# Kernel tuning notes

Measured on AMD Instinct MI355X. Metric: run time of the kernel, lower is better.

The kernel has to match this reference:

```python
import jax, jax.numpy as jnp
import numpy as np

# ---- model dims ----
D_MODEL = 256; D_STATE = 128; D_CONV = 4; EXPAND = 2; HEADDIM = 64
D_INNER = EXPAND * D_MODEL            # 512
NHEADS = D_INNER // HEADDIM           # 8
CONV_DIM = D_INNER + 2 * D_STATE      # 768
D_IN_PROJ = 2 * D_INNER + 2 * D_STATE + NHEADS  # 1288
N_GENES = 4095; BATCH = 4; CHUNK = 64
GENE_ID_DIM = 64; PATH_DIM = 128; CHR_DIM = 16; N_CHROM = 25; LFF = 32
GENE_FEAT_DIM = GENE_ID_DIM + PATH_DIM + 2 * CHR_DIM  # 224
N_PERT = 2048; PERT_DIM = 128


def silu(x):
    return x * jax.nn.sigmoid(x)


def segsum_exp(a):
    # a: (..., T). Returns lower-triangular exp(sum_{k=j+1..i} a_k), zero above diag.
    T = a.shape[-1]
    cs = jnp.cumsum(a, axis=-1)
    d = cs[..., :, None] - cs[..., None, :]
    mask = jnp.tril(jnp.ones((T, T), dtype=bool))
    return jnp.exp(jnp.where(mask, d, 0.0)) * mask


def ssd(X, A, B, C):
    # Chunked SSD (Mamba2 selective scan). X:(b,l,h,p) pre-multiplied by dt,
    # A:(b,l,h) = a*dt, B/C:(b,l,n) (ngroups=1 broadcast over heads).
    b, l, h, p = X.shape
    n = B.shape[-1]
    c = l // CHUNK
    Xc = X.reshape(b, c, CHUNK, h, p)
    Bc = B.reshape(b, c, CHUNK, n)
    Cc = C.reshape(b, c, CHUNK, n)
    Ac = A.reshape(b, c, CHUNK, h).transpose(0, 3, 1, 2)  # (b,h,c,cl)
    A_cs = jnp.cumsum(Ac, axis=-1)
    L = segsum_exp(Ac)                                     # (b,h,c,cl,cl)
    Y_diag = jnp.einsum('bcln,bcsn,bhcls,bcshp->bclhp', Cc, Bc, L, Xc)
    decay_states = jnp.exp(A_cs[..., -1:] - A_cs)          # (b,h,c,cl)
    states = jnp.einsum('bcln,bhcl,bclhp->bchpn', Bc, decay_states, Xc)
    chunk_decay = jnp.exp(A_cs[..., -1])                   # (b,h,c)

    def step(h_prev, inp):
        dec, s = inp
        return h_prev * dec[..., None, None] + s, h_prev

    init = jnp.zeros((b, h, p, n), X.dtype)
    _, prev = jax.lax.scan(step, init, (chunk_decay.transpose(2, 0, 1),
                                        states.transpose(1, 0, 2, 3, 4)))
    prev = prev.transpose(1, 0, 2, 3, 4)                   # (b,c,h,p,n)
    Y_off = jnp.einsum('bcln,bchpn,bhcl->bclhp', Cc, prev, jnp.exp(A_cs))
    return (Y_diag + Y_off).reshape(b, l, h, p)


def mamba2(x, in_w, conv_w, conv_b, dt_bias, A_log, D, norm_w, out_w):
    b, l, _ = x.shape
    zxbcdt = x @ in_w.T                                    # (b,l,1288)
    z = zxbcdt[..., :D_INNER]
    xBC = zxbcdt[..., D_INNER:D_INNER + CONV_DIM]
    dt = jax.nn.softplus(zxbcdt[..., D_INNER + CONV_DIM:] + dt_bias)  # (b,l,h)
    # causal depthwise conv1d
    xc = jax.lax.conv_general_dilated(
        xBC.transpose(0, 2, 1), conv_w[:, None, :], (1,), [(D_CONV - 1, 0)],
        feature_group_count=CONV_DIM,
        dimension_numbers=('NCH', 'OIH', 'NCH'))
    xBC = silu(xc.transpose(0, 2, 1) + conv_b)
    xs = xBC[..., :D_INNER].reshape(b, l, NHEADS, HEADDIM)
    Bm = xBC[..., D_INNER:D_INNER + D_STATE]
    Cm = xBC[..., D_INNER + D_STATE:]
    A = -jnp.exp(A_log)                                    # (h,)
    y = ssd(xs * dt[..., None], dt * A, Bm, Cm) + D[:, None] * xs
    y = y.reshape(b, l, D_INNER)
    y = y * silu(z)                                        # gated RMSNorm
    y = y * jax.lax.rsqrt(jnp.mean(y * y, axis=-1, keepdims=True) + 1e-5) * norm_w
    return y @ out_w.T


def _forward(perturbation_idx, chr_idx, locus_fourier, pathway_features,
             gene_id_emb, chr_emb, locus_w, locus_b, pert_emb, cond_w, cond_b,
             inp_w, inp_b, ln_g, ln_b,
             mf_in_w, mf_conv_w, mf_conv_b, mf_dt_bias, mf_A_log, mf_D, mf_norm_w, mf_out_w,
             mb_in_w, mb_conv_w, mb_conv_b, mb_dt_bias, mb_A_log, mb_D, mb_norm_w, mb_out_w,
             head_w, head_b):
    e_locus = jax.nn.gelu(locus_fourier @ locus_w.T + locus_b, approximate=False)
    gene_feat = jnp.concatenate(
        [gene_id_emb, pathway_features, chr_emb[chr_idx], e_locus], axis=-1)  # (G,224)
    cond = pert_emb[perturbation_idx] @ cond_w.T + cond_b                      # (B,224)
    seq = jnp.concatenate(
        [cond[:, None, :],
         jnp.broadcast_to(gene_feat[None], (BATCH, N_GENES, GENE_FEAT_DIM))], axis=1)
    seq = seq @ inp_w.T + inp_b                                                # (B,4096,256)
    mu = jnp.mean(seq, axis=-1, keepdims=True)
    var = jnp.var(seq, axis=-1, keepdims=True)
    seq = (seq - mu) * jax.lax.rsqrt(var + 1e-5) * ln_g + ln_b
    # L = 4096 is already a multiple of 16 -> no padding branch.
    h_fwd = mamba2(seq, mf_in_w, mf_conv_w, mf_conv_b, mf_dt_bias, mf_A_log, mf_D, mf_norm_w, mf_out_w)
    h_bwd = jnp.flip(mamba2(jnp.flip(seq, 1), mb_in_w, mb_conv_w, mb_conv_b, mb_dt_bias, mb_A_log, mb_D, mb_norm_w, mb_out_w), 1)
    H = h_fwd + h_bwd
    return H[:, 1:, :] @ head_w.T + head_b                                     # (B,4095,1)


def setup_inputs() -> dict:
    key = jax.random.key(0)
    ks = iter(jax.random.split(key, 64))

    def nrm(shape, s=0.02):
        return jax.random.normal(next(ks), shape, jnp.float32) * s

    inp = {}
    inp['perturbation_idx'] = jax.random.randint(next(ks), (BATCH,), 0, N_PERT)
    inp['chr_idx'] = jax.random.randint(next(ks), (N_GENES,), 0, N_CHROM)
    inp['locus_fourier'] = nrm((N_GENES, 2 * LFF), 1.0)
    inp['pathway_features'] = nrm((N_GENES, PATH_DIM), 1.0)
    inp['gene_id_emb'] = nrm((N_GENES, GENE_ID_DIM))
    inp['chr_emb'] = nrm((N_CHROM, CHR_DIM))
    inp['locus_w'] = nrm((CHR_DIM, 2 * LFF)); inp['locus_b'] = jnp.zeros((CHR_DIM,))
    inp['pert_emb'] = nrm((N_PERT, PERT_DIM))
    inp['cond_w'] = nrm((GENE_FEAT_DIM, PERT_DIM)); inp['cond_b'] = jnp.zeros((GENE_FEAT_DIM,))
    inp['inp_w'] = nrm((D_MODEL, GENE_FEAT_DIM)); inp['inp_b'] = jnp.zeros((D_MODEL,))
    inp['ln_g'] = jnp.ones((D_MODEL,)); inp['ln_b'] = jnp.zeros((D_MODEL,))
    for pre in ('mf_', 'mb_'):
        inp[pre + 'in_w'] = nrm((D_IN_PROJ, D_MODEL))
        inp[pre + 'conv_w'] = nrm((CONV_DIM, D_CONV), 0.2)
        inp[pre + 'conv_b'] = jnp.zeros((CONV_DIM,))
        inp[pre + 'dt_bias'] = nrm((NHEADS,), 0.5)
        inp[pre + 'A_log'] = jnp.log(jax.random.uniform(next(ks), (NHEADS,), jnp.float32, 1.0, 16.0))
        inp[pre + 'D'] = jnp.ones((NHEADS,))
        inp[pre + 'norm_w'] = jnp.ones((D_INNER,))
        inp[pre + 'out_w'] = nrm((D_MODEL, D_INNER))
    inp['head_w'] = nrm((1, D_MODEL)); inp['head_b'] = jnp.zeros((1,))
    return inp


def reference(perturbation_idx, chr_idx, locus_fourier, pathway_features,
              gene_id_emb, chr_emb, locus_w, locus_b, pert_emb, cond_w, cond_b,
              inp_w, inp_b, ln_g, ln_b,
              mf_in_w, mf_conv_w, mf_conv_b, mf_dt_bias, mf_A_log, mf_D, mf_norm_w, mf_out_w,
              mb_in_w, mb_conv_w, mb_conv_b, mb_dt_bias, mb_A_log, mb_D, mb_norm_w, mb_out_w,
              head_w, head_b):
    return _forward(perturbation_idx, chr_idx, locus_fourier, pathway_features,
                    gene_id_emb, chr_emb, locus_w, locus_b, pert_emb, cond_w, cond_b,
                    inp_w, inp_b, ln_g, ln_b,
                    mf_in_w, mf_conv_w, mf_conv_b, mf_dt_bias, mf_A_log, mf_D, mf_norm_w, mf_out_w,
                    mb_in_w, mb_conv_w, mb_conv_b, mb_dt_bias, mb_A_log, mb_D, mb_norm_w, mb_out_w,
                    head_w, head_b)
```

## Files before the change

kernel.cpp:

```cpp
#include <hip/hip_runtime.h>
#include <hip/hip_bf16.h>
#include <math.h>

#define LSEQ   4096
#define NGENES 4095
#define NB     4
#define DM     256
#define DI     512
#define DST    128
#define NH     8
#define HD     64
#define CONVD  768
#define DIP    1288
#define NCHK   64
#define CHK    64
#define GFD    224

#define ZN  ((size_t)NB*LSEQ*DI)
#define XN  ((size_t)NB*LSEQ*CONVD)
#define DN  ((size_t)NB*LSEQ*NH)
#define AN  ((size_t)NB*NH*LSEQ)
#define SN  ((size_t)NB*NCHK*NH*HD*DST)
#define GN  ((size_t)NB*NCHK*CHK*CHK)
#define BTN ((size_t)NB*NCHK*DST*CHK)
#define HN  ((size_t)NB*LSEQ*DM)

typedef short bf16x8 __attribute__((ext_vector_type(8)));
typedef short bf16x4 __attribute__((ext_vector_type(4)));
typedef float f32x4 __attribute__((ext_vector_type(4)));

__device__ __forceinline__ float bf2f(unsigned short u){
    unsigned int x = ((unsigned int)u) << 16;
    return __uint_as_float(x);
}
__device__ __forceinline__ unsigned short f2bf(float f){
    __hip_bfloat16 h = __float2bfloat16(f);
    return *reinterpret_cast<unsigned short*>(&h);
}

typedef const __attribute__((address_space(1))) void* gas_t;
typedef __attribute__((address_space(3))) void* las_t;
__device__ __forceinline__ void gload16(const void* g, void* l){
    __builtin_amdgcn_global_load_lds((gas_t)g, (las_t)l, 16, 0, 0);
}

__global__ void k_detect(const unsigned int* p, int* flag){
    *flag = (*p == 0x3F803F80u) ? 1 : 0;
}

struct ConvAll { const void* src[31]; float* dst[31]; int n[31]; };
__global__ void k_convert_all(ConvAll a, const int* flag){
    int ai = blockIdx.y;
    int n = a.n[ai];
    const void* s = a.src[ai]; float* d = a.dst[ai];
    bool bf = (*flag != 0);
    for(int i = blockIdx.x*256 + threadIdx.x; i < n; i += gridDim.x*256){
        d[i] = bf ? bf2f(((const unsigned short*)s)[i]) : ((const float*)s)[i];
    }
}

struct PackAll { const void* src[4]; unsigned short* dst[4]; int n[4]; };
__global__ void k_pack_all(PackAll a, const int* flag){
    int ai = blockIdx.y;
    int n = a.n[ai];
    const void* s = a.src[ai]; unsigned short* d = a.dst[ai];
    bool bf = (*flag != 0);
    for(int i = blockIdx.x*256 + threadIdx.x; i < n; i += gridDim.x*256){
        if(bf) d[i] = ((const unsigned short*)s)[i];
        else   d[i] = f2bf(((const float*)s)[i]);
    }
}

__global__ void k_packw256(const void* src, unsigned short* dst, const int* flag){
    int row = blockIdx.x, col = threadIdx.x;
    unsigned short v = 0;
    if(col < GFD){
        if(*flag) v = ((const unsigned short*)src)[row*GFD + col];
        else      v = f2bf(((const float*)src)[row*GFD + col]);
    }
    dst[row*256 + col] = v;
}

__global__ void k_genefeat(const float* gene_id, const float* pathway, const float* chr_emb,
                           const int* chr_idx, const float* lf, const float* locus_w,
                           const float* locus_b, unsigned short* gfb){
    int g = blockIdx.x; int t = threadIdx.x;
    float v = 0.f;
    if(t < 64)       v = gene_id[g*64 + t];
    else if(t < 192) v = pathway[g*128 + (t-64)];
    else if(t < 208) v = chr_emb[chr_idx[g]*16 + (t-192)];
    else if(t < 224){
        int j = t - 208;
        float acc = locus_b[j];
        for(int k=0;k<64;k++) acc += lf[g*64+k]*locus_w[j*64+k];
        v = 0.5f*acc*(1.0f + erff(acc*0.7071067811865475f));
    }
    gfb[g*256 + t] = f2bf(v);
}

__global__ void k_cond(const int* pidx, const float* pert_emb, const float* cond_w,
                       const float* cond_b, unsigned short* condb){
    int b = blockIdx.x, t = threadIdx.x;
    float acc = 0.f;
    if(t < GFD){
        const float* pe = pert_emb + pidx[b]*128;
        acc = cond_b[t];
        for(int k=0;k<128;k++) acc += pe[k]*cond_w[t*128+k];
    }
    condb[b*256 + t] = f2bf(acc);
}

__global__ __launch_bounds__(256) void k_mm_seqpre(const unsigned short* gfb,
            const unsigned short* condb, const unsigned short* Wb,
            const float* inp_b, float* seq_pre){
    __shared__ unsigned short sh[16384];
    int sblk = (blockIdx.x & 7)*32 + (blockIdx.x >> 3);
    int bm = sblk>>1, bn = sblk&1;
    int m0 = bm*128, n0 = bn*128;
    int t = threadIdx.x, lane = t&63;
    int wid = t>>6, wm = wid>>1, wn = wid&1;
    int fr = lane&15, fk = lane>>4;
    int srow = t>>3;
    int scol = ((t&7) ^ (srow&7))*8;
    const unsigned short* gA[4]; const unsigned short* gB[4];
#pragma unroll
    for(int q=0;q<4;q++){
        int row = q*32 + srow;
        int m = m0+row; int b = m>>12, l = m&4095;
        gA[q] = l ? &gfb[(size_t)(l-1)*256 + scol] : &condb[(size_t)b*256 + scol];
        gB[q] = &Wb[(size_t)(n0+row)*256 + scol];
    }
    unsigned short* lA = &sh[t*8];
    unsigned short* lB = &sh[8192 + t*8];
    f32x4 acc[4][4];
#pragma unroll
    for(int i=0;i<4;i++)
#pragma unroll
        for(int j=0;j<4;j++) acc[i][j] = (f32x4){0.f,0.f,0.f,0.f};
    for(int it=0; it<4; it++){
#pragma unroll
        for(int q=0;q<4;q++){
            gload16(gA[q], lA + q*2048);
            gload16(gB[q], lB + q*2048);
            gA[q] += 64; gB[q] += 64;
        }
        __syncthreads();
#pragma unroll
        for(int kk8=0;kk8<8;kk8+=4){
            bf16x8 av[4], bv[4];
#pragma unroll
            for(int i=0;i<4;i++){
                int r = wm*64+i*16+fr;
                av[i] = *(bf16x8*)&sh[r*64 + (((kk8+fk)^(r&7))*8)];
            }
#pragma unroll
            for(int j=0;j<4;j++){
                int r = wn*64+j*16+fr;
                bv[j] = *(bf16x8*)&sh[8192 + r*64 + (((kk8+fk)^(r&7))*8)];
            }
#pragma unroll
            for(int i=0;i<4;i++)
#pragma unroll
                for(int j=0;j<4;j++)
                    acc[i][j] = __builtin_amdgcn_mfma_f32_16x16x32_bf16(av[i], bv[j], acc[i][j], 0,0,0);
        }
        __syncthreads();
    }
#pragma unroll
    for(int i=0;i<4;i++)
#pragma unroll
        for(int rr=0;rr<4;rr++){
            int m = m0 + wm*64 + i*16 + fk*4 + rr;
#pragma unroll
            for(int j=0;j<4;j++){
                int n = n0 + wn*64 + j*16 + fr;
                seq_pre[(size_t)m*256 + n] = acc[i][j][rr] + inp_b[n];
            }
        }
}

__global__ void k_ln(const float* seq_pre, const float* ln_g, const float* ln_b,
                     unsigned short* seqb){
    int t = threadIdx.x; int w = t>>6, lane = t&63;
    int m = blockIdx.x*4 + w;
    f32x4 v = *(const f32x4*)&seq_pre[(size_t)m*256 + lane*4];
    float s1 = v[0]+v[1]+v[2]+v[3];
    float s2 = v[0]*v[0]+v[1]*v[1]+v[2]*v[2]+v[3]*v[3];
#pragma unroll
    for(int o=32;o>0;o>>=1){ s1 += __shfl_xor(s1,o,64); s2 += __shfl_xor(s2,o,64); }
    float mu  = s1*(1.f/256.f);
    float var = s2*(1.f/256.f) - mu*mu;
    float rs = rsqrtf(var+1e-5f);
    unsigned short o4[4];
#pragma unroll
    for(int j=0;j<4;j++){
        int n = lane*4+j;
        o4[j] = f2bf((v[j]-mu)*rs*ln_g[n] + ln_b[n]);
    }
    *(unsigned long long*)&seqb[(size_t)m*256 + lane*4] = *(unsigned long long*)o4;
}

__global__ __launch_bounds__(256) void k_mm_inproj(const unsigned short* seqb,
            const unsigned short* W0, const unsigned short* W1,
            const float* dtb0, const float* dtb1,
            unsigned short* zbase, unsigned short* xbase, float* dtbase){
    __shared__ unsigned short sh[16384];
    int blk = (blockIdx.x & 7)*352 + (blockIdx.x >> 3);
    int dir = blk >= 1408; int inner = blk - dir*1408;
    int bm = inner/11, bn = inner%11;
    int m0 = bm*128, n0 = bn*128;
    const unsigned short* Wb = dir ? W1 : W0;
    const float* dt_bias = dir ? dtb1 : dtb0;
    unsigned short* zb   = zbase + (size_t)dir*ZN;
    unsigned short* xbcr = xbase + (size_t)dir*XN;
    float* dtb = dtbase + (size_t)dir*DN;
    int t = threadIdx.x, lane = t&63;
    int wid = t>>6, wm = wid>>1, wn = wid&1;
    int fr = lane&15, fk = lane>>4;
    int srow = t>>3;
    int scol = ((t&7) ^ (srow&7))*8;
    const unsigned short* gA[4]; const unsigned short* gB[4];
#pragma unroll
    for(int q=0;q<4;q++){
        int row = q*32 + srow;
        int m = m0+row; int b = m>>12, l = m&4095;
        int ml = dir ? (4095-l) : l;
        gA[q] = &seqb[(size_t)(b*4096+ml)*256 + scol];
        gB[q] = &Wb[(size_t)(n0+row)*256 + scol];
    }
    unsigned short* lA = &sh[t*8];
    unsigned short* lB = &sh[8192 + t*8];
    f32x4 acc[4][4];
#pragma unroll
    for(int i=0;i<4;i++)
#pragma unroll
        for(int j=0;j<4;j++) acc[i][j] = (f32x4){0.f,0.f,0.f,0.f};
    for(int it=0; it<4; it++){
#pragma unroll
        for(int q=0;q<4;q++){
            gload16(gA[q], lA + q*2048);
            gload16(gB[q], lB + q*2048);
            gA[q] += 64; gB[q] += 64;
        }
        __syncthreads();
#pragma unroll
        for(int kk8=0;kk8<8;kk8+=4){
            bf16x8 av[4], bv[4];
#pragma unroll
            for(int i=0;i<4;i++){
                int r = wm*64+i*16+fr;
                av[i] = *(bf16x8*)&sh[r*64 + (((kk8+fk)^(r&7))*8)];
            }
#pragma unroll
            for(int j=0;j<4;j++){
                int r = wn*64+j*16+fr;
                bv[j] = *(bf16x8*)&sh[8192 + r*64 + (((kk8+fk)^(r&7))*8)];
            }
#pragma unroll
            for(int i=0;i<4;i++)
#pragma unroll
                for(int j=0;j<4;j++)
                    acc[i][j] = __builtin_amdgcn_mfma_f32_16x16x32_bf16(av[i], bv[j], acc[i][j], 0,0,0);
        }
        __syncthreads();
    }
    if(bn == 10){
#pragma unroll
        for(int i=0;i<4;i++)
#pragma unroll
            for(int rr=0;rr<4;rr++){
                int m = m0 + wm*64 + i*16 + fk*4 + rr;
#pragma unroll
                for(int j=0;j<4;j++){
                    int n = n0 + wn*64 + j*16 + fr;
                    if(n >= DIP) continue;
                    int hh = n - 1280;
                    float x = acc[i][j][rr] + dt_bias[hh];
                    dtb[(size_t)m*NH + hh] = (x > 20.f) ? x : log1pf(expf(x));
                }
            }
        return;
    }
    unsigned short* dst; int stride, coff;
    if(bn < 4){ dst = zb;   stride = DI;    coff = bn*128; }
    else      { dst = xbcr; stride = CONVD; coff = bn*128 - 512; }
#pragma unroll
    for(int p=0;p<2;p++){
        if(wm == p){
#pragma unroll
            for(int i=0;i<4;i++)
#pragma unroll
                for(int j=0;j<4;j++)
#pragma unroll
                    for(int rr=0;rr<4;rr++){
                        int row = i*16 + fk*4 + rr;
                        int col = wn*64 + j*16 + fr;
                        sh[row*136 + col] = f2bf(acc[i][j][rr]);
                    }
        }
        __syncthreads();
#pragma unroll
        for(int k=0;k<4;k++){
            int idx = t + k*256;
            int row = idx>>4, c8 = (idx&15)*8;
            bf16x8 v = *(bf16x8*)&sh[row*136 + c8];
            *(bf16x8*)&dst[(size_t)(m0+p*64+row)*stride + coff + c8] = v;
        }
        __syncthreads();
    }
}

__global__ __launch_bounds__(256) void k_conv(const unsigned short* xbase,
        const float* cw0, const float* cw1, const float* cb0, const float* cb1,
        unsigned short* obase){
    __shared__ unsigned short raw[19*768];
    __shared__ float cwf[4*768];
    __shared__ float cbf[768];
    int blk = blockIdx.x;
    int dir = blk>>10; int rem = blk&1023;
    int b = rem>>8, rg = rem&255;
    const unsigned short* xr = xbase + (size_t)dir*XN;
    unsigned short* out = obase + (size_t)dir*XN;
    const float* cw = dir ? cw1 : cw0;
    const float* cb = dir ? cb1 : cb0;
    int l0 = rg*16;
    int t = threadIdx.x;
    for(int i=t;i<3072;i+=256){ int q=i/768, c=i%768; cwf[q*768+c] = cw[c*4+q]; }
    for(int i=t;i<768;i+=256) cbf[i] = cb[i];
    for(int i=t;i<19*96;i+=256){
        int r = i/96, c8 = (i%96)*8;
        int l = l0 - 3 + r;
        bf16x8 v = (bf16x8){0,0,0,0,0,0,0,0};
        if(l >= 0) v = *(const bf16x8*)&xr[(size_t)(b*4096+l)*768 + c8];
        *(bf16x8*)&raw[r*768 + c8] = v;
    }
    __syncthreads();
    for(int i=t;i<16*96;i+=256){
        int r = i/96, c8 = (i%96)*8;
        bf16x8 o;
#pragma unroll
        for(int j=0;j<8;j++){
            int c = c8+j;
            float acc = cbf[c];
#pragma unroll
            for(int q=0;q<4;q++) acc += cwf[q*768+c]*bf2f(raw[(r+q)*768 + c]);
            o[j] = (short)f2bf(acc/(1.f+expf(-acc)));
        }
        *(bf16x8*)&out[(size_t)(b*4096+l0+r)*768 + c8] = o;
    }
}

__global__ void k_cumsum(const float* dtbase, const float* Al0, const float* Al1,
                         float* acsbase){
    __shared__ float tmp[64];
    int blk = blockIdx.x;
    int dir = blk>>11; int rem = blk&2047;
    int c = rem & 63; int bh = rem >> 6; int h = bh & 7; int b = bh >> 3;
    const float* dtb = dtbase + (size_t)dir*DN;
    float* acs = acsbase + (size_t)dir*AN;
    int s = threadIdx.x;
    float A = -expf((dir?Al1:Al0)[h]);
    int l = c*64 + s;
    tmp[s] = dtb[(size_t)(b*4096+l)*NH + h] * A;
    __syncthreads();
    if(s == 0){ for(int i=1;i<64;i++) tmp[i] += tmp[i-1]; }
    __syncthreads();
    acs[(size_t)(b*8+h)*4096 + l] = tmp[s];
}

__global__ __launch_bounds__(256) void k_cbprep(const unsigned short* xbase,
        unsigned short* Gbase, unsigned short* BTbase){
    __shared__ unsigned short Bb[64][136];
    __shared__ unsigned short Cb[64][136];
    __shared__ unsigned short BTs[128][72];
    int blk = blockIdx.x;
    int dir = blk>>8; int bc = blk&255;
    int b = bc>>6, c = bc&63;
    const unsigned short* xbcb = xbase + (size_t)dir*XN;
    unsigned short* Gb = Gbase + (size_t)dir*GN;
    unsigned short* BTg = BTbase + (size_t)dir*BTN;
    int t = threadIdx.x, lane = t&63, wid = t>>6;
    int fr = lane&15, fk = lane>>4;
    size_t rowbase = (size_t)(b*4096 + c*64)*CONVD;
#pragma unroll
    for(int q=0;q<4;q++){
        int e = t + q*256; int r = e>>4, ch = (e&15)*8;
        *(bf16x8*)&Bb[r][ch] = *(const bf16x8*)&xbcb[rowbase + (size_t)r*CONVD + 512 + ch];
        *(bf16x8*)&Cb[r][ch] = *(const bf16x8*)&xbcb[rowbase + (size_t)r*CONVD + 640 + ch];
    }
    __syncthreads();
    f32x4 g[4];
#pragma unroll
    for(int j=0;j<4;j++) g[j] = (f32x4){0.f,0.f,0.f,0.f};
#pragma unroll
    for(int k0=0;k0<128;k0+=32){
        bf16x8 av = *(bf16x8*)&Cb[wid*16+fr][k0+fk*8];
#pragma unroll
        for(int j=0;j<4;j++){
            bf16x8 bv = *(bf16x8*)&Bb[j*16+fr][k0+fk*8];
            g[j] = __builtin_amdgcn_mfma_f32_16x16x32_bf16(av, bv, g[j], 0,0,0);
        }
    }
    size_t gbase = (size_t)bc*4096;
#pragma unroll
    for(int j=0;j<4;j++)
#pragma unroll
        for(int rr=0;rr<4;rr++)
            Gb[gbase + (size_t)(wid*16+fk*4+rr)*64 + j*16+fr] = f2bf(g[j][rr]);
#pragma unroll
    for(int q=0;q<4;q++){
        int e = t + q*256; int s = e>>4, n0 = (e&15)*8;
        bf16x8 v = *(bf16x8*)&Bb[s][n0];
#pragma unroll
        for(int j=0;j<8;j++){
            int n = n0 + j;
            BTs[n][s ^ (n&56)] = (unsigned short)v[j];
        }
    }
    __syncthreads();
    size_t btbase = (size_t)bc*8192;
#pragma unroll
    for(int q=0;q<4;q++){
        int e = t + q*256; int n = e>>3, s0 = (e&7)*8;
        bf16x8 v = *(bf16x8*)&BTs[n][s0 ^ (n&56)];
        *(bf16x8*)&BTg[btbase + (size_t)n*64 + s0] = v;
    }
}

__global__ __launch_bounds__(256) void k_ssd_intra(const unsigned short* xbase,
        const unsigned short* Gbase, const unsigned short* BTbase,
        const float* dtbase, const float* acsbase,
        const float* Dv0, const float* Dv1,
        unsigned short* Ybase, unsigned short* sbase_){
    __shared__ unsigned short Gs[64][72];
    __shared__ unsigned short Ms[64][72];
    __shared__ unsigned short XT[64][72];
    __shared__ unsigned short BTs[128][72];
    __shared__ float acs_s[64], dts[64], ws[64];
    int blk = blockIdx.x;
    int dir = blk>>9; int rem = blk&511;
    int hg = rem&1, c = (rem>>1)&63, b = rem>>7;
    int bc = b*64 + c;
    const unsigned short* xbcb = xbase + (size_t)dir*XN;
    const unsigned short* Gb = Gbase + (size_t)dir*GN;
    const unsigned short* BTg = BTbase + (size_t)dir*BTN;
    const float* dtb = dtbase + (size_t)dir*DN;
    const float* acs = acsbase + (size_t)dir*AN;
    const float* Dv = dir ? Dv1 : Dv0;
    unsigned short* Yb = Ybase + (size_t)dir*XN;
    unsigned short* states = sbase_ + (size_t)dir*SN;
    int t = threadIdx.x, lane = t&63, wid = t>>6;
    int wr = wid>>1, wc = wid&1;
    int fr = lane&15, fk = lane>>4;
    size_t rowbase = (size_t)(b*4096 + c*64)*CONVD;
    size_t gbase = (size_t)bc*4096;
    size_t btbase = (size_t)bc*8192;
#pragma unroll
    for(int q=0;q<2;q++){
        int e = t + q*256; int l = e>>3, s0 = (e&7)*8;
        *(bf16x8*)&Gs[l][s0] = *(const bf16x8*)&Gb[gbase + (size_t)l*64 + s0];
    }
#pragma unroll
    for(int q=0;q<4;q++){
        int e = t + q*256; int n = e>>3, s0 = (e&7)*8;
        *(bf16x8*)&BTs[n][s0 ^ (n&56)] = *(const bf16x8*)&BTg[btbase + (size_t)n*64 + s0];
    }
    for(int hh=0; hh<4; hh++){
        int h = hg*4 + hh;
        __syncthreads();
#pragma unroll
        for(int q=0;q<2;q++){
            int e = t + q*256; int s = e>>3, p0 = (e&7)*8;
            bf16x8 v = *(const bf16x8*)&xbcb[rowbase + (size_t)s*CONVD + h*64 + p0];
            int sw = s ^ (p0&56);
#pragma unroll
            for(int j=0;j<8;j++) XT[p0+j][sw] = (unsigned short)v[j];
        }
        if(t < 64){
            acs_s[t] = acs[(size_t)(b*8+h)*4096 + c*64 + t];
            dts[t]   = dtb[(size_t)(b*4096 + c*64 + t)*NH + h];
        }
        __syncthreads();
        if(t < 64) ws[t] = expf(acs_s[63]-acs_s[t])*dts[t];
#pragma unroll
        for(int q=0;q<16;q++){
            int e = t + q*256; int l = e>>6, s = e&63;
            float m = (s <= l) ? bf2f(Gs[l][s])*expf(acs_s[l]-acs_s[s])*dts[s] : 0.f;
            Ms[l][s] = f2bf(m);
        }
        __syncthreads();
        f32x4 y[2][2];
#pragma unroll
        for(int i=0;i<2;i++)
#pragma unroll
            for(int j=0;j<2;j++) y[i][j] = (f32x4){0.f,0.f,0.f,0.f};
#pragma unroll
        for(int k0=0;k0<64;k0+=32){
            bf16x8 av[2], bv[2];
#pragma unroll
            for(int i=0;i<2;i++) av[i] = *(bf16x8*)&Ms[wr*32+i*16+fr][k0+fk*8];
#pragma unroll
            for(int j=0;j<2;j++){
                int p = wc*32+j*16+fr;
                bv[j] = *(bf16x8*)&XT[p][(k0+fk*8) ^ (p&56)];
            }
#pragma unroll
            for(int i=0;i<2;i++)
#pragma unroll
                for(int j=0;j<2;j++)
                    y[i][j] = __builtin_amdgcn_mfma_f32_16x16x32_bf16(av[i], bv[j], y[i][j], 0,0,0);
        }
        float Dh = Dv[h];
#pragma unroll
        for(int i=0;i<2;i++)
#pragma unroll
            for(int j=0;j<2;j++)
#pragma unroll
                for(int rr=0;rr<4;rr++){
                    int l = wr*32 + i*16 + fk*4 + rr;
                    int p = wc*32 + j*16 + fr;
                    float xv = bf2f(XT[p][l ^ (p&56)]);
                    Yb[(size_t)(b*4096 + c*64 + l)*DI + h*64 + p] = f2bf(y[i][j][rr] + Dh*xv);
                }
        f32x4 s4[2][4];
#pragma unroll
        for(int i=0;i<2;i++)
#pragma unroll
            for(int j=0;j<4;j++) s4[i][j] = (f32x4){0.f,0.f,0.f,0.f};
#pragma unroll
        for(int k0=0;k0<64;k0+=32){
            bf16x8 av[2], bv[4];
#pragma unroll
            for(int i=0;i<2;i++){
                int p = wr*32+i*16+fr;
                bf16x8 raw = *(bf16x8*)&XT[p][(k0+fk*8) ^ (p&56)];
#pragma unroll
                for(int e=0;e<8;e++) av[i][e] = (short)f2bf(bf2f((unsigned short)raw[e]) * ws[k0+fk*8+e]);
            }
#pragma unroll
            for(int j=0;j<4;j++){
                int n = wc*64+j*16+fr;
                bv[j] = *(bf16x8*)&BTs[n][(k0+fk*8) ^ (n&56)];
            }
#pragma unroll
            for(int i=0;i<2;i++)
#pragma unroll
                for(int j=0;j<4;j++)
                    s4[i][j] = __builtin_amdgcn_mfma_f32_16x16x32_bf16(av[i], bv[j], s4[i][j], 0,0,0);
        }
        size_t sb = ((size_t)bc*8 + h)*8192;
#pragma unroll
        for(int i=0;i<2;i++)
#pragma unroll
            for(int j=0;j<4;j++)
#pragma unroll
                for(int rr=0;rr<4;rr++){
                    int p = wr*32 + i*16 + fk*4 + rr;
                    int n = wc*64 + j*16 + fr;
                    states[sb + p*128 + n] = f2bf(s4[i][j][rr]);
                }
    }
}

__global__ void k_scan(unsigned short* sbase_, const float* acsbase){
    __shared__ float dec_s[64];
    int blk = blockIdx.x;
    int dir = blk>>8; int rem = blk&255;
    int e8 = rem&7, h = (rem>>3)&7, b = rem>>6;
    unsigned short* states = sbase_ + (size_t)dir*SN;
    const float* acs = acsbase + (size_t)dir*AN;
    int t = threadIdx.x;
    if(t < 64) dec_s[t] = expf(acs[(size_t)(b*8+h)*4096 + t*64 + 63]);
    __syncthreads();
    int off = e8*1024 + t*4;
    float h4[4] = {0.f,0.f,0.f,0.f};
    size_t base0 = ((size_t)(b*64)*8 + h)*8192 + off;
    for(int c0=0;c0<64;c0+=4){
        bf16x4 v[4];
#pragma unroll
        for(int u=0;u<4;u++)
            v[u] = *(const bf16x4*)&states[base0 + (size_t)(c0+u)*65536];
#pragma unroll
        for(int u=0;u<4;u++){
            float dec = dec_s[c0+u];
            bf16x4 o;
#pragma unroll
            for(int j=0;j<4;j++){
                o[j] = (short)f2bf(h4[j]);
                h4[j] = h4[j]*dec + bf2f((unsigned short)v[u][j]);
            }
            *(bf16x4*)&states[base0 + (size_t)(c0+u)*65536] = o;
        }
    }
}

__global__ __launch_bounds__(256) void k_ssd_off(const unsigned short* xbase,
        const unsigned short* sbase_, const float* acsbase, unsigned short* Ybase){
    __shared__ unsigned short Ct[64][136];
    __shared__ unsigned short Pv[64][136];
    __shared__ float acs_s[64];
    int blk = blockIdx.x;
    int dir = blk>>8; int bc = blk&255;
    int c = bc&63, b = bc>>6;
    const unsigned short* xbcb = xbase + (size_t)dir*XN;
    const unsigned short* prev = sbase_ + (size_t)dir*SN;
    const float* acs = acsbase + (size_t)dir*AN;
    unsigned short* Yb = Ybase + (size_t)dir*XN;
    int t = threadIdx.x, lane = t&63, wid = t>>6;
    int wr = wid>>1, wc = wid&1;
    int fr = lane&15, fk = lane>>4;
    size_t rowbase = (size_t)(b*4096 + c*64)*CONVD;
#pragma unroll
    for(int q=0;q<4;q++){
        int e = t + q*256;
        int r = e>>4, ch = (e&15)*8;
        *(bf16x8*)&Ct[r][ch] = *(const bf16x8*)&xbcb[rowbase + (size_t)r*CONVD + 640 + ch];
    }
    for(int h=0; h<8; h++){
        size_t sb = ((size_t)bc*8 + h)*8192;
        __syncthreads();
#pragma unroll
        for(int q=0;q<4;q++){
            int e = t + q*256;
            int r = e>>4, ch = (e&15)*8;
            *(bf16x8*)&Pv[r][ch] = *(const bf16x8*)&prev[sb + (size_t)r*128 + ch];
        }
        if(t < 64) acs_s[t] = acs[(size_t)(b*8+h)*4096 + c*64 + t];
        __syncthreads();
        f32x4 o[2][2];
#pragma unroll
        for(int i=0;i<2;i++)
#pragma unroll
            for(int j=0;j<2;j++) o[i][j] = (f32x4){0.f,0.f,0.f,0.f};
        for(int k0=0;k0<128;k0+=32){
            bf16x8 av[2], bv[2];
#pragma unroll
            for(int i=0;i<2;i++) av[i] = *(bf16x8*)&Ct[wr*32+i*16+fr][k0+fk*8];
#pragma unroll
            for(int j=0;j<2;j++) bv[j] = *(bf16x8*)&Pv[wc*32+j*16+fr][k0+fk*8];
#pragma unroll
            for(int i=0;i<2;i++)
#pragma unroll
                for(int j=0;j<2;j++)
                    o[i][j] = __builtin_amdgcn_mfma_f32_16x16x32_bf16(av[i], bv[j], o[i][j], 0,0,0);
        }
#pragma unroll
        for(int i=0;i<2;i++)
#pragma unroll
            for(int j=0;j<2;j++)
#pragma unroll
                for(int rr=0;rr<4;rr++){
                    int l = wr*32 + i*16 + fk*4 + rr;
                    int p = wc*32 + j*16 + fr;
                    size_t yi = (size_t)(b*4096 + c*64 + l)*DI + h*64 + p;
                    float cur = bf2f(Yb[yi]);
                    Yb[yi] = f2bf(cur + o[i][j][rr]*expf(acs_s[l]));
                }
    }
}

__global__ void k_gate(const unsigned short* Ybase, const unsigned short* zbase,
                       const float* nw0, const float* nw1, unsigned short* ynbase){
    int blk = blockIdx.x;
    int dir = blk>>12;
    int t = threadIdx.x; int w = t>>6, lane = t&63;
    int m = (blk&4095)*4 + w;
    const unsigned short* Yb = Ybase + (size_t)dir*XN;
    const unsigned short* zb = zbase + (size_t)dir*ZN;
    unsigned short* ynb = ynbase + (size_t)dir*SN;
    const float* norm_w = dir ? nw1 : nw0;
    size_t base = (size_t)m*DI + lane*8;
    bf16x8 yv = *(const bf16x8*)&Yb[base];
    bf16x8 zv = *(const bf16x8*)&zb[base];
    float v[8]; float ss = 0.f;
#pragma unroll
    for(int j=0;j<8;j++){
        float zf = bf2f((unsigned short)zv[j]);
        float f = bf2f((unsigned short)yv[j]) * (zf/(1.f+expf(-zf)));
        v[j] = f; ss += f*f;
    }
#pragma unroll
    for(int o=32;o>0;o>>=1) ss += __shfl_xor(ss,o,64);
    float r = rsqrtf(ss*(1.f/512.f) + 1e-5f);
    bf16x8 o8;
#pragma unroll
    for(int j=0;j<8;j++) o8[j] = (short)f2bf(v[j]*r*norm_w[lane*8+j]);
    *(bf16x8*)&ynb[base] = o8;
}

__global__ __launch_bounds__(256) void k_mm_outproj(const unsigned short* ynbase,
            const unsigned short* W0, const unsigned short* W1, float* Hbase){
    __shared__ unsigned short sh[16384];
    int blk = (blockIdx.x & 7)*64 + (blockIdx.x >> 3);
    int dir = blk>>8; int rem = blk&255;
    int bm = rem>>1, bn = rem&1;
    int m0 = bm*128, n0 = bn*128;
    const unsigned short* ynb = ynbase + (size_t)dir*SN;
    const unsigned short* Wb = dir ? W1 : W0;
    float* H = Hbase + (size_t)dir*HN;
    int t = threadIdx.x, lane = t&63;
    int wid = t>>6, wm = wid>>1, wn = wid&1;
    int fr = lane&15, fk = lane>>4;
    int srow = t>>3;
    int scol = ((t&7) ^ (srow&7))*8;
    const unsigned short* gA[4]; const unsigned short* gB[4];
#pragma unroll
    for(int q=0;q<4;q++){
        int row = q*32 + srow;
        gA[q] = &ynb[(size_t)(m0+row)*512 + scol];
        gB[q] = &Wb[(size_t)(n0+row)*512 + scol];
    }
    unsigned short* lA = &sh[t*8];
    unsigned short* lB = &sh[8192 + t*8];
    f32x4 acc[4][4];
#pragma unroll
    for(int i=0;i<4;i++)
#pragma unroll
        for(int j=0;j<4;j++) acc[i][j] = (f32x4){0.f,0.f,0.f,0.f};
    for(int it=0; it<8; it++){
#pragma unroll
        for(int q=0;q<4;q++){
            gload16(gA[q], lA + q*2048);
            gload16(gB[q], lB + q*2048);
            gA[q] += 64; gB[q] += 64;
        }
        __syncthreads();
#pragma unroll
        for(int kk8=0;kk8<8;kk8+=4){
            bf16x8 av[4], bv[4];
#pragma unroll
            for(int i=0;i<4;i++){
                int r = wm*64+i*16+fr;
                av[i] = *(bf16x8*)&sh[r*64 + (((kk8+fk)^(r&7))*8)];
            }
#pragma unroll
            for(int j=0;j<4;j++){
                int r = wn*64+j*16+fr;
                bv[j] = *(bf16x8*)&sh[8192 + r*64 + (((kk8+fk)^(r&7))*8)];
            }
#pragma unroll
            for(int i=0;i<4;i++)
#pragma unroll
                for(int j=0;j<4;j++)
                    acc[i][j] = __builtin_amdgcn_mfma_f32_16x16x32_bf16(av[i], bv[j], acc[i][j], 0,0,0);
        }
        __syncthreads();
    }
#pragma unroll
    for(int i=0;i<4;i++)
#pragma unroll
        for(int rr=0;rr<4;rr++){
            int m = m0 + wm*64 + i*16 + fk*4 + rr;
            int b = m>>12, l = m&4095;
            int ml = dir ? (4095 - l) : l;
#pragma unroll
            for(int j=0;j<4;j++){
                int n = n0 + wn*64 + j*16 + fr;
                H[(size_t)(b*4096+ml)*256 + n] = acc[i][j][rr];
            }
        }
}

__global__ void k_head(const float* H0, const float* H1, const float* head_w,
                       const float* head_b, void* out, const int* flag){
    int t = threadIdx.x; int w = t>>6, lane = t&63;
    int row = blockIdx.x*4 + w;
    int b = row/4095, g = row - b*4095;
    size_t idx = ((size_t)(b*4096) + g + 1)*256 + lane*4;
    f32x4 h0 = *(const f32x4*)&H0[idx];
    f32x4 h1 = *(const f32x4*)&H1[idx];
    f32x4 wv = *(const f32x4*)&head_w[lane*4];
    float ss = (h0[0]+h1[0])*wv[0]+(h0[1]+h1[1])*wv[1]+(h0[2]+h1[2])*wv[2]+(h0[3]+h1[3])*wv[3];
#pragma unroll
    for(int o=32;o>0;o>>=1) ss += __shfl_xor(ss,o,64);
    if(lane == 0){
        float val = ss + head_b[0];
        if(*flag) ((__hip_bfloat16*)out)[b*4095 + g] = __float2bfloat16(val);
        else      ((float*)out)[b*4095 + g] = val;
    }
}

extern "C" void kernel_launch(void* const* d_in, const int* in_sizes, int n_in,
                              void* d_out, int out_size, void* d_ws, size_t ws_size,
                              hipStream_t stream){
    if(n_in < 33){
        hipMemsetAsync(d_out, 0, (size_t)out_size*2, stream);
        return;
    }
    char* base = (char*)d_ws;
    size_t off = 256;
    int* flag = (int*)base;
    auto alloc = [&](size_t nbytes)->char*{
        char* p = base + off;
        off += ((nbytes + 255) & ~(size_t)255);
        return p;
    };
    float* F[33];
    for(int i=0;i<33;i++){
        if(i==0 || i==1 || i==11 || i==15 || i==22 || i==23 || i==30){ F[i] = nullptr; continue; }
        F[i] = (float*)alloc((size_t)in_sizes[i]*4);
    }
    unsigned short* inwb[2];
    unsigned short* outwb[2];
    inwb[0]  = (unsigned short*)alloc((size_t)DIP*DM*2);
    inwb[1]  = (unsigned short*)alloc((size_t)DIP*DM*2);
    outwb[0] = (unsigned short*)alloc((size_t)DM*DI*2);
    outwb[1] = (unsigned short*)alloc((size_t)DM*DI*2);
    unsigned short* inpwb = (unsigned short*)alloc((size_t)DM*256*2);
    unsigned short* gfb   = (unsigned short*)alloc((size_t)NGENES*256*2);
    unsigned short* condb = (unsigned short*)alloc((size_t)NB*256*2);
    unsigned short* seqb  = (unsigned short*)alloc((size_t)NB*LSEQ*DM*2);
    float* H0      = (float*)alloc(HN*4);
    float* H1      = (float*)alloc(HN*4);
    unsigned short* zb   = (unsigned short*)alloc(ZN*2*2);
    unsigned short* xbcr = (unsigned short*)alloc(XN*2*2);
    unsigned short* xbcb = (unsigned short*)alloc(XN*2*2);
    float* dtb     = (float*)alloc(DN*2*4);
    float* acs     = (float*)alloc(AN*2*4);
    unsigned short* states = (unsigned short*)alloc(SN*2*2);
    unsigned short* Gb  = (unsigned short*)H0;
    unsigned short* BTg = (unsigned short*)((char*)H0 + ((GN*2*2 + 255) & ~(size_t)255));
    float* seq_pre = (float*)xbcr;
    unsigned short* Ybuf = xbcr;
    unsigned short* ynb = states;
    if(off > ws_size){
        hipMemsetAsync(d_out, 0, (size_t)out_size*2, stream);
        return;
    }

    k_detect<<<1,1,0,stream>>>((const unsigned int*)d_in[13], flag);

    ConvAll ca;
    for(int i=2;i<33;i++){
        int ai = i-2;
        ca.src[ai] = d_in[i];
        ca.dst[ai] = F[i];
        int n = in_sizes[i];
        if(i==11 || i==15 || i==22 || i==23 || i==30) n = 0;
        ca.n[ai] = n;
    }
    k_convert_all<<<dim3(96,31),256,0,stream>>>(ca, flag);

    PackAll pa;
    pa.src[0] = d_in[15]; pa.dst[0] = inwb[0];  pa.n[0] = DIP*DM;
    pa.src[1] = d_in[23]; pa.dst[1] = inwb[1];  pa.n[1] = DIP*DM;
    pa.src[2] = d_in[22]; pa.dst[2] = outwb[0]; pa.n[2] = DM*DI;
    pa.src[3] = d_in[30]; pa.dst[3] = outwb[1]; pa.n[3] = DM*DI;
    k_pack_all<<<dim3(64,4),256,0,stream>>>(pa, flag);
    k_packw256<<<DM,256,0,stream>>>(d_in[11], inpwb, flag);

    k_genefeat<<<NGENES,256,0,stream>>>(F[4], F[3], F[5], (const int*)d_in[1],
                                        F[2], F[6], F[7], gfb);
    k_cond<<<NB,256,0,stream>>>((const int*)d_in[0], F[8], F[9], F[10], condb);
    k_mm_seqpre<<<128*2,256,0,stream>>>(gfb, condb, inpwb, F[12], seq_pre);
    k_ln<<<NB*LSEQ/4,256,0,stream>>>(seq_pre, F[13], F[14], seqb);

    k_mm_inproj<<<2816,256,0,stream>>>(seqb, inwb[0], inwb[1], F[18], F[26],
                                       zb, xbcr, dtb);
    k_conv<<<2048,256,0,stream>>>(xbcr, F[16], F[24], F[17], F[25], xbcb);
    k_cumsum<<<4096,64,0,stream>>>(dtb, F[19], F[27], acs);
    k_cbprep<<<512,256,0,stream>>>(xbcb, Gb, BTg);
    k_ssd_intra<<<1024,256,0,stream>>>(xbcb, Gb, BTg, dtb, acs, F[20], F[28],
                                       Ybuf, states);
    k_scan<<<512,256,0,stream>>>(states, acs);
    k_ssd_off<<<512,256,0,stream>>>(xbcb, states, acs, Ybuf);
    k_gate<<<8192,256,0,stream>>>(Ybuf, zb, F[21], F[29], ynb);
    k_mm_outproj<<<512,256,0,stream>>>(ynb, outwb[0], outwb[1], H0);

    k_head<<<NB*NGENES/4,256,0,stream>>>(H0, H1, F[31], F[32], d_out, flag);
}
```

Before: 285.0 us.

## Coalesce SSD output stores via LDS and move off-diagonal add into gate

Stages the intra-chunk Y and chunk-state outputs in a single shared buffer so global writes become coalesced 16-byte stores. The off-diagonal kernel writes its term into the now-dead x region of the conv buffer instead of read-modify-writing Y, and the gate kernel sums both terms. Also switches several expf calls to fast __expf. It adds barriers and reuses conv buffer space, and relies on x no longer being needed after the intra kernel.

```diff
diff --git a/kernel.cpp b/kernel.cpp
--- a/kernel.cpp
+++ b/kernel.cpp
@@ -344,7 +344,7 @@
             float acc = cbf[c];
 #pragma unroll
             for(int q=0;q<4;q++) acc += cwf[q*768+c]*bf2f(raw[(r+q)*768 + c]);
-            o[j] = (short)f2bf(acc/(1.f+expf(-acc)));
+            o[j] = (short)f2bf(acc/(1.f+__expf(-acc)));
         }
         *(bf16x8*)&out[(size_t)(b*4096+l0+r)*768 + c8] = o;
     }
@@ -427,15 +427,16 @@
     }
 }
 
+#define G_OFF  0
+#define BT_OFF 4608
+#define XT_OFF 13824
+#define MS_OFF 18432
 __global__ __launch_bounds__(256) void k_ssd_intra(const unsigned short* xbase,
         const unsigned short* Gbase, const unsigned short* BTbase,
         const float* dtbase, const float* acsbase,
         const float* Dv0, const float* Dv1,
         unsigned short* Ybase, unsigned short* sbase_){
-    __shared__ unsigned short Gs[64][72];
-    __shared__ unsigned short Ms[64][72];
-    __shared__ unsigned short XT[64][72];
-    __shared__ unsigned short BTs[128][72];
+    __shared__ unsigned short sh[23040];
     __shared__ float acs_s[64], dts[64], ws[64];
     int blk = blockIdx.x;
     int dir = blk>>9; int rem = blk&511;
@@ -458,12 +459,12 @@
 #pragma unroll
     for(int q=0;q<2;q++){
         int e = t + q*256; int l = e>>3, s0 = (e&7)*8;
-        *(bf16x8*)&Gs[l][s0] = *(const bf16x8*)&Gb[gbase + (size_t)l*64 + s0];
+        *(bf16x8*)&sh[G_OFF + l*72 + s0] = *(const bf16x8*)&Gb[gbase + (size_t)l*64 + s0];
     }
 #pragma unroll
     for(int q=0;q<4;q++){
         int e = t + q*256; int n = e>>3, s0 = (e&7)*8;
-        *(bf16x8*)&BTs[n][s0 ^ (n&56)] = *(const bf16x8*)&BTg[btbase + (size_t)n*64 + s0];
+        *(bf16x8*)&sh[BT_OFF + n*72 + (s0 ^ (n&56))] = *(const bf16x8*)&BTg[btbase + (size_t)n*64 + s0];
     }
     for(int hh=0; hh<4; hh++){
         int h = hg*4 + hh;
@@ -474,19 +475,19 @@
             bf16x8 v = *(const bf16x8*)&xbcb[rowbase + (size_t)s*CONVD + h*64 + p0];
             int sw = s ^ (p0&56);
 #pragma unroll
-            for(int j=0;j<8;j++) XT[p0+j][sw] = (unsigned short)v[j];
+            for(int j=0;j<8;j++) sh[XT_OFF + (p0+j)*72 + sw] = (unsigned short)v[j];
         }
         if(t < 64){
             acs_s[t] = acs[(size_t)(b*8+h)*4096 + c*64 + t];
             dts[t]   = dtb[(size_t)(b*4096 + c*64 + t)*NH + h];
         }
         __syncthreads();
-        if(t < 64) ws[t] = expf(acs_s[63]-acs_s[t])*dts[t];
+        if(t < 64) ws[t] = __expf(acs_s[63]-acs_s[t])*dts[t];
 #pragma unroll
         for(int q=0;q<16;q++){
             int e = t + q*256; int l = e>>6, s = e&63;
-            float m = (s <= l) ? bf2f(Gs[l][s])*expf(acs_s[l]-acs_s[s])*dts[s] : 0.f;
-            Ms[l][s] = f2bf(m);
+            float m = (s <= l) ? bf2f(sh[G_OFF + l*72 + s])*__expf(acs_s[l]-acs_s[s])*dts[s] : 0.f;
+            sh[MS_OFF + l*72 + s] = f2bf(m);
         }
         __syncthreads();
         f32x4 y[2][2];
@@ -498,11 +499,11 @@
         for(int k0=0;k0<64;k0+=32){
             bf16x8 av[2], bv[2];
 #pragma unroll
-            for(int i=0;i<2;i++) av[i] = *(bf16x8*)&Ms[wr*32+i*16+fr][k0+fk*8];
+            for(int i=0;i<2;i++) av[i] = *(bf16x8*)&sh[MS_OFF + (wr*32+i*16+fr)*72 + k0+fk*8];
 #pragma unroll
             for(int j=0;j<2;j++){
                 int p = wc*32+j*16+fr;
-                bv[j] = *(bf16x8*)&XT[p][(k0+fk*8) ^ (p&56)];
+                bv[j] = *(bf16x8*)&sh[XT_OFF + p*72 + ((k0+fk*8) ^ (p&56))];
             }
 #pragma unroll
             for(int i=0;i<2;i++)
@@ -510,6 +511,7 @@
                 for(int j=0;j<2;j++)
                     y[i][j] = __builtin_amdgcn_mfma_f32_16x16x32_bf16(av[i], bv[j], y[i][j], 0,0,0);
         }
+        __syncthreads();
         float Dh = Dv[h];
 #pragma unroll
         for(int i=0;i<2;i++)
@@ -519,8 +521,8 @@
                 for(int rr=0;rr<4;rr++){
                     int l = wr*32 + i*16 + fk*4 + rr;
                     int p = wc*32 + j*16 + fr;
-                    float xv = bf2f(XT[p][l ^ (p&56)]);
-                    Yb[(size_t)(b*4096 + c*64 + l)*DI + h*64 + p] = f2bf(y[i][j][rr] + Dh*xv);
+                    float xv = bf2f(sh[XT_OFF + p*72 + (l ^ (p&56))]);
+                    sh[MS_OFF + l*72 + p] = f2bf(y[i][j][rr] + Dh*xv);
                 }
         f32x4 s4[2][4];
 #pragma unroll
@@ -533,14 +535,14 @@
 #pragma unroll
             for(int i=0;i<2;i++){
                 int p = wr*32+i*16+fr;
-                bf16x8 raw = *(bf16x8*)&XT[p][(k0+fk*8) ^ (p&56)];
+                bf16x8 raw = *(bf16x8*)&sh[XT_OFF + p*72 + ((k0+fk*8) ^ (p&56))];
 #pragma unroll
                 for(int e=0;e<8;e++) av[i][e] = (short)f2bf(bf2f((unsigned short)raw[e]) * ws[k0+fk*8+e]);
             }
 #pragma unroll
             for(int j=0;j<4;j++){
                 int n = wc*64+j*16+fr;
-                bv[j] = *(bf16x8*)&BTs[n][(k0+fk*8) ^ (n&56)];
+                bv[j] = *(bf16x8*)&sh[BT_OFF + n*72 + ((k0+fk*8) ^ (n&56))];
             }
 #pragma unroll
             for(int i=0;i<2;i++)
@@ -548,7 +550,14 @@
                 for(int j=0;j<4;j++)
                     s4[i][j] = __builtin_amdgcn_mfma_f32_16x16x32_bf16(av[i], bv[j], s4[i][j], 0,0,0);
         }
-        size_t sb = ((size_t)bc*8 + h)*8192;
+        __syncthreads();
+#pragma unroll
+        for(int k=0;k<2;k++){
+            int e = t + k*256; int row = e>>3, c8 = (e&7)*8;
+            bf16x8 v = *(bf16x8*)&sh[MS_OFF + row*72 + c8];
+            *(bf16x8*)&Yb[(size_t)(b*4096 + c*64 + row)*DI + h*64 + c8] = v;
+        }
+        __syncthreads();
 #pragma unroll
         for(int i=0;i<2;i++)
 #pragma unroll
@@ -557,8 +566,16 @@
                 for(int rr=0;rr<4;rr++){
                     int p = wr*32 + i*16 + fk*4 + rr;
                     int n = wc*64 + j*16 + fr;
-                    states[sb + p*128 + n] = f2bf(s4[i][j][rr]);
+                    sh[XT_OFF + p*128 + (n ^ ((p&7)<<3))] = f2bf(s4[i][j][rr]);
                 }
+        __syncthreads();
+        size_t sb = ((size_t)bc*8 + h)*8192;
+#pragma unroll
+        for(int k=0;k<4;k++){
+            int e = t + k*256; int p = e>>4, c8 = (e&15)*8;
+            bf16x8 v = *(bf16x8*)&sh[XT_OFF + p*128 + (c8 ^ ((p&7)<<3))];
+            *(bf16x8*)&states[sb + p*128 + c8] = v;
+        }
     }
 }
 
@@ -570,7 +587,7 @@
     unsigned short* states = sbase_ + (size_t)dir*SN;
     const float* acs = acsbase + (size_t)dir*AN;
     int t = threadIdx.x;
-    if(t < 64) dec_s[t] = expf(acs[(size_t)(b*8+h)*4096 + t*64 + 63]);
+    if(t < 64) dec_s[t] = __expf(acs[(size_t)(b*8+h)*4096 + t*64 + 63]);
     __syncthreads();
     int off = e8*1024 + t*4;
     float h4[4] = {0.f,0.f,0.f,0.f};
@@ -594,22 +611,22 @@
     }
 }
 
-__global__ __launch_bounds__(256) void k_ssd_off(const unsigned short* xbase,
-        const unsigned short* sbase_, const float* acsbase, unsigned short* Ybase){
+__global__ __launch_bounds__(256) void k_ssd_off(unsigned short* xbase,
+        const unsigned short* sbase_, const float* acsbase){
     __shared__ unsigned short Ct[64][136];
     __shared__ unsigned short Pv[64][136];
     __shared__ float acs_s[64];
     int blk = blockIdx.x;
     int dir = blk>>8; int bc = blk&255;
     int c = bc&63, b = bc>>6;
-    const unsigned short* xbcb = xbase + (size_t)dir*XN;
+    unsigned short* xbcb = xbase + (size_t)dir*XN;
     const unsigned short* prev = sbase_ + (size_t)dir*SN;
     const float* acs = acsbase + (size_t)dir*AN;
-    unsigned short* Yb = Ybase + (size_t)dir*XN;
     int t = threadIdx.x, lane = t&63, wid = t>>6;
     int wr = wid>>1, wc = wid&1;
     int fr = lane&15, fk = lane>>4;
     size_t rowbase = (size_t)(b*4096 + c*64)*CONVD;
+    unsigned short* ostg = &Pv[0][0];
 #pragma unroll
     for(int q=0;q<4;q++){
         int e = t + q*256;
@@ -644,6 +661,7 @@
                 for(int j=0;j<2;j++)
                     o[i][j] = __builtin_amdgcn_mfma_f32_16x16x32_bf16(av[i], bv[j], o[i][j], 0,0,0);
         }
+        __syncthreads();
 #pragma unroll
         for(int i=0;i<2;i++)
 #pragma unroll
@@ -652,31 +670,40 @@
                 for(int rr=0;rr<4;rr++){
                     int l = wr*32 + i*16 + fk*4 + rr;
                     int p = wc*32 + j*16 + fr;
-                    size_t yi = (size_t)(b*4096 + c*64 + l)*DI + h*64 + p;
-                    float cur = bf2f(Yb[yi]);
-                    Yb[yi] = f2bf(cur + o[i][j][rr]*expf(acs_s[l]));
+                    ostg[l*72 + p] = f2bf(o[i][j][rr]*__expf(acs_s[l]));
                 }
-    }
-}
-
-__global__ void k_gate(const unsigned short* Ybase, const unsigned short* zbase,
+        __syncthreads();
+#pragma unroll
+        for(int k=0;k<2;k++){
+            int e = t + k*256; int row = e>>3, c8 = (e&7)*8;
+            bf16x8 v = *(bf16x8*)&ostg[row*72 + c8];
+            *(bf16x8*)&xbcb[rowbase + (size_t)row*CONVD + h*64 + c8] = v;
+        }
+    }
+}
+
+__global__ void k_gate(const unsigned short* Ybase, const unsigned short* xbase,
+                       const unsigned short* zbase,
                        const float* nw0, const float* nw1, unsigned short* ynbase){
     int blk = blockIdx.x;
     int dir = blk>>12;
     int t = threadIdx.x; int w = t>>6, lane = t&63;
     int m = (blk&4095)*4 + w;
     const unsigned short* Yb = Ybase + (size_t)dir*XN;
+    const unsigned short* Ob = xbase + (size_t)dir*XN;
     const unsigned short* zb = zbase + (size_t)dir*ZN;
     unsigned short* ynb = ynbase + (size_t)dir*SN;
     const float* norm_w = dir ? nw1 : nw0;
     size_t base = (size_t)m*DI + lane*8;
     bf16x8 yv = *(const bf16x8*)&Yb[base];
+    bf16x8 ov = *(const bf16x8*)&Ob[(size_t)m*CONVD + lane*8];
     bf16x8 zv = *(const bf16x8*)&zb[base];
     float v[8]; float ss = 0.f;
 #pragma unroll
     for(int j=0;j<8;j++){
         float zf = bf2f((unsigned short)zv[j]);
-        float f = bf2f((unsigned short)yv[j]) * (zf/(1.f+expf(-zf)));
+        float yt = bf2f((unsigned short)yv[j]) + bf2f((unsigned short)ov[j]);
+        float f = yt * (zf/(1.f+__expf(-zf)));
         v[j] = f; ss += f*f;
     }
 #pragma unroll
@@ -863,8 +890,8 @@
     k_ssd_intra<<<1024,256,0,stream>>>(xbcb, Gb, BTg, dtb, acs, F[20], F[28],
                                        Ybuf, states);
     k_scan<<<512,256,0,stream>>>(states, acs);
-    k_ssd_off<<<512,256,0,stream>>>(xbcb, states, acs, Ybuf);
-    k_gate<<<8192,256,0,stream>>>(Ybuf, zb, F[21], F[29], ynb);
+    k_ssd_off<<<512,256,0,stream>>>(xbcb, states, acs);
+    k_gate<<<8192,256,0,stream>>>(Ybuf, xbcb, zb, F[21], F[29], ynb);
     k_mm_outproj<<<512,256,0,stream>>>(ynb, outwb[0], outwb[1], H0);
 
     k_head<<<NB*NGENES/4,256,0,stream>>>(H0, H1, F[31], F[32], d_out, flag);
```

Result: no change. 280.4 us (-1.6%).
